# Optimization experiments

Hardware: AMD Instinct MI355X
Metric: run time of the kernel (lower is better)

The kernel has to match this reference:

```python
import jax, jax.numpy as jnp
import numpy as np

P = 8      # patch_size
DIM = 16   # per-head channel dim
HEADS = 4
LN_EPS = 1e-6


def _conv_patch(x, W, b):
    # stride=kernel=P patch conv; SAME degenerates to VALID when H%P==0
    y = jax.lax.conv_general_dilated(
        x, W, window_strides=(P, P), padding='VALID',
        dimension_numbers=('NHWC', 'HWIO', 'NHWC'))
    return y + b


def _proj_heads(x, W, b):
    # b h w (c p0 p1 head) -> b head (h p0) (w p1) c
    y = _conv_patch(x, W, b)
    B, hh, ww, _ = y.shape
    y = y.reshape(B, hh, ww, DIM, P, P, HEADS)
    y = y.transpose(0, 6, 1, 4, 2, 5, 3)            # b head hh p0 ww p1 c
    return y.reshape(B, HEADS, hh * P, ww * P, DIM)


def _to_patch(t):
    # n head (h p1) (w p2) c -> n head c h w p1 p2
    B, hd, H, W, c = t.shape
    t = t.reshape(B, hd, H // P, P, W // P, P, c)
    return t.transpose(0, 1, 6, 2, 4, 3, 5)


def _from_patch(t):
    # n head c h w p1 p2 -> n head (h p1) (w p2) c
    B, hd, c, hh, ww, _, _ = t.shape
    t = t.transpose(0, 1, 3, 5, 4, 6, 2)
    return t.reshape(B, hd, hh * P, ww * P, c)


def setup_inputs() -> dict:
    key = jax.random.key(0)
    ks = jax.random.split(key, 6)
    B, H, W, Cin = 4, 256, 256, 16
    feat = DIM * HEADS * P * P  # 4096
    s_qkv = 0.02
    inp = {
        'x': jax.random.normal(ks[0], (B, H, W, Cin), jnp.float32),
        'Wq': jax.random.normal(ks[1], (P, P, Cin, feat), jnp.float32) * s_qkv,
        'bq': jnp.zeros((feat,), jnp.float32),
        'Wk': jax.random.normal(ks[2], (P, P, Cin, feat), jnp.float32) * s_qkv,
        'bk': jnp.zeros((feat,), jnp.float32),
        'Wv': jax.random.normal(ks[3], (P, P, Cin, feat), jnp.float32) * s_qkv,
        'bv': jnp.zeros((feat,), jnp.float32),
        'ln_scale': jnp.ones((DIM,), jnp.float32),
        'ln_bias': jnp.zeros((DIM,), jnp.float32),
        'Wout': jax.random.normal(ks[4], (P, P, HEADS * DIM, DIM * P * P), jnp.float32) * 0.02,
        'bout': jnp.zeros((DIM * P * P,), jnp.float32),
    }
    return inp


def reference(x, Wq, bq, Wk, bk, Wv, bv, ln_scale, ln_bias, Wout, bout):
    q = _proj_heads(x, Wq, bq)  # [B, heads, H, W, dim]
    k = _proj_heads(x, Wk, bk)
    v = _proj_heads(x, Wv, bv)

    # frequency-domain 'attention': per-8x8-patch rfft2 multiply irfft2
    qf = jnp.fft.rfft2(_to_patch(q))
    kf = jnp.fft.rfft2(_to_patch(k))
    out = jnp.fft.irfft2(qf * kf, s=(P, P))
    out = _from_patch(out)                          # [B, heads, H, W, dim]

    # LayerNorm over channel dim (flax default eps=1e-6, scale+bias)
    mu = out.mean(-1, keepdims=True)
    var = ((out - mu) ** 2).mean(-1, keepdims=True)
    out = (out - mu) * jax.lax.rsqrt(var + LN_EPS) * ln_scale + ln_bias

    out = v * out
    # b head h w c -> b h w (head c)
    B, hd, H, W, c = out.shape
    out = out.transpose(0, 2, 3, 1, 4).reshape(B, H, W, hd * c)

    # output projection (no heads): conv then b h w (c p0 p1) -> b (h p0) (w p1) c
    y = _conv_patch(out, Wout, bout)
    Bo, hh, ww, _ = y.shape
    y = y.reshape(Bo, hh, ww, DIM, P, P).transpose(0, 1, 4, 2, 5, 3)
    return y.reshape(Bo, hh * P, ww * P, DIM)
```

## Files before the change

kernel.cpp:

```cpp
#include <hip/hip_runtime.h>
#include <hip/hip_bf16.h>
#include <cstdint>
#include <cstddef>

typedef float  f32x4  __attribute__((ext_vector_type(4)));
typedef __bf16 bf16x8 __attribute__((ext_vector_type(8)));
typedef __bf16 bf16x4 __attribute__((ext_vector_type(4)));


#define GLOAD_LDS16(gp, lp)                                                     \
    __builtin_amdgcn_global_load_lds(                                           \
        (const __attribute__((address_space(1))) void*)(gp),                    \
        (__attribute__((address_space(3))) void*)(lp), 16, 0, 0)

#define MFMA16(d, a, b) d = __builtin_amdgcn_mfma_f32_16x16x32_bf16(a, b, d, 0, 0, 0)

#define BAR() asm volatile("s_barrier" ::: "memory")

__global__ __launch_bounds__(256) void k_im2col(const float* __restrict__ x,
                                                __bf16* __restrict__ Xb)
{
    const int p = blockIdx.x;
    const int t = threadIdx.x;
    const int b = p >> 10, hh = (p >> 5) & 31, ww = p & 31;
    const int e = t * 4;
    const int c = e & 15, ij = e >> 4;
    const int i = ij >> 3, j = ij & 7;
    const size_t src = ((((size_t)(b * 256 + hh * 8 + i)) * 256) + (ww * 8 + j)) * 16 + c;
    f32x4 v = *(const f32x4*)(x + src);
    bf16x4 o;
    o[0] = (__bf16)v[0]; o[1] = (__bf16)v[1]; o[2] = (__bf16)v[2]; o[3] = (__bf16)v[3];
    *(bf16x4*)(Xb + (size_t)p * 1024 + e) = o;
}

__global__ __launch_bounds__(256) void k_wqkvT(const float* __restrict__ Wq,
                                               const float* __restrict__ Wk,
                                               const float* __restrict__ Wv,
                                               __bf16* __restrict__ WT)
{
    __shared__ float tile[64][261];
    int q = blockIdx.x;
    const int t = threadIdx.x;
    const int kb = q & 15;   q >>= 4;
    const int ch = q & 15;   q >>= 4;
    const int s  = q;
    const int k0 = kb * 64;
    const float* __restrict__ W = (s == 0) ? Wq : (s == 1) ? Wk : Wv;

#pragma unroll
    for (int rep = 0; rep < 16; rep++) {
        const int idx = rep * 256 + t;
        const int kl = idx >> 6, col4 = (idx & 63) * 4;
        const f32x4 v = *(const f32x4*)(W + (size_t)(k0 + kl) * 4096 + ch * 256 + col4);
        tile[kl][col4 + 0] = v[0];
        tile[kl][col4 + 1] = v[1];
        tile[kl][col4 + 2] = v[2];
        tile[kl][col4 + 3] = v[3];
    }
    __syncthreads();
    const size_t nbase = (size_t)s * 4096 + ch * 64;
#pragma unroll
    for (int rep = 0; rep < 64; rep++) {
        const int idx = rep * 256 + t;
        const int kl = idx & 63;
        const int rest = idx >> 6;
        const int p = rest & 63, h = rest >> 6;
        WT[(nbase + h * 1024 + p) * 1024 + k0 + kl] = (__bf16)tile[kl][p * 4 + h];
    }
}

__global__ __launch_bounds__(256) void k_biasperm(const float* __restrict__ bq,
                                                  const float* __restrict__ bk,
                                                  const float* __restrict__ bv,
                                                  float* __restrict__ bp)
{
    const int n = blockIdx.x * 256 + threadIdx.x;
    const int s = n >> 12;
    const int r = n & 4095;
    const int head = r >> 10, c = (r >> 6) & 15, pp = r & 63;
    const float* __restrict__ b = (s == 0) ? bq : (s == 1) ? bk : bv;
    bp[n] = b[c * 256 + pp * 4 + head];
}

__global__ __launch_bounds__(256) void k_woutT(const float* __restrict__ Wo,
                                               __bf16* __restrict__ WT)
{
    __shared__ float tile[64][129];
    const int q = blockIdx.x;
    const int t = threadIdx.x;
    const int n0 = (q & 15) * 64;
    const int k0 = (q >> 4) * 128;
    const int ch = n0 >> 6;
#pragma unroll
    for (int rep = 0; rep < 32; rep++) {
        const int idx = rep * 256 + t;
        const int kl = idx >> 6, nn = idx & 63;
        tile[nn][kl] = Wo[(size_t)(k0 + kl) * 1024 + n0 + nn];
    }
    __syncthreads();
#pragma unroll
    for (int rep = 0; rep < 32; rep++) {
        const int idx = rep * 256 + t;
        const int nn = idx >> 7, kl = idx & 127;
        const int no = ((nn >> 3) & 7) * 128 + (nn & 7) * 16 + ch;
        WT[(size_t)no * 4096 + k0 + kl] = (__bf16)tile[nn][kl];
    }
}

__device__ __forceinline__ void stage_half(const __bf16* __restrict__ mat,
                                           const int gRow0, const int K,
                                           const int k0, __bf16* lds, const int t)
{
    const int w6 = (t >> 6) << 6;
#pragma unroll
    for (int r = 0; r < 2; r++) {
        const int idx = r * 512 + t;
        const int row = idx >> 3;
        const int colb = ((t & 7) << 4) ^ ((row & 7) << 4);
        const char* gp = (const char*)(mat + (size_t)(gRow0 + row) * K + k0) + colb;
        GLOAD_LDS16(gp, (char*)lds + (size_t)(r * 512 + w6) * 16);
    }
}

__global__ __launch_bounds__(512, 1) void gemm256(const __bf16* __restrict__ A,
                                                  const __bf16* __restrict__ Bt,
                                                  __bf16* __restrict__ C,
                                                  const float* __restrict__ bias,
                                                  const int M, const int N,
                                                  const int K, const int nby)
{
    __shared__ __bf16 As[2][256 * 64];
    __shared__ __bf16 Bs[2][256 * 64];

    const int t = threadIdx.x;
    const int l = t & 63, w = t >> 6;
    const int wr = w >> 2, wc = w & 3;

    const int nwg = (int)gridDim.x, cpx = nwg >> 3;
    const int bid = (int)blockIdx.x;
    const int sbid = (bid & 7) * cpx + (bid >> 3);
    const int bm = sbid % nby, bn = sbid / nby;
    const int row0 = bm * 256, col0 = bn * 256;

    const int lrow = l & 15;
    const int lkb  = (l >> 4) << 4;
    const int lswz = (l & 7) << 4;
    const int ce0 = ((0  + lkb) ^ lswz) >> 1;
    const int ce1 = ((64 + lkb) ^ lswz) >> 1;

    const int arow = wr * 128 + lrow;
    const int brow = wc * 64 + lrow;

    const int NT = K >> 6;
    f32x4 acc[8][4] = {};
    bf16x8 a0[4][2], a1[4][2], b0[2][2], b1[2][2];

    stage_half(A,  row0,       K, 0,  As[0],        t);
    stage_half(A,  row0 + 128, K, 0,  As[0] + 8192, t);
    stage_half(A,  row0,       K, 64, As[1],        t);
    stage_half(A,  row0 + 128, K, 64, As[1] + 8192, t);
    stage_half(Bt, col0,       K, 0,  Bs[0],        t);
    stage_half(Bt, col0 + 128, K, 0,  Bs[0] + 8192, t);
    asm volatile("s_waitcnt vmcnt(0)" ::: "memory");
    BAR();
#pragma unroll
    for (int mi = 0; mi < 4; ++mi) {
        const int rr = (arow + mi * 16) * 64;
        a0[mi][0] = *(const bf16x8*)&As[0][rr + ce0];
        a0[mi][1] = *(const bf16x8*)&As[0][rr + ce1];
    }

    int cur = 0;
    for (int it = 0; it < NT; ++it) {
        const __bf16* AsC = As[cur];
        const __bf16* AsN = As[cur ^ 1];
        const __bf16* BsC = Bs[cur];
        __bf16* BsN = Bs[cur ^ 1];
        const bool stB = (it + 1 < NT);
        const bool stA = (it + 2 < NT);
        const bool pfA = (it + 1 < NT);
        const int kB = (it + 1) << 6;
        const int kA = (it + 2) << 6;

        BAR();
#pragma unroll
        for (int ni = 0; ni < 2; ++ni) {
            const int rr = (brow + ni * 16) * 64;
            b0[ni][0] = *(const bf16x8*)&BsC[rr + ce0];
            b0[ni][1] = *(const bf16x8*)&BsC[rr + ce1];
        }
#pragma unroll
        for (int ni = 0; ni < 2; ++ni) {
            const int rr = (brow + 32 + ni * 16) * 64;
            b1[ni][0] = *(const bf16x8*)&BsC[rr + ce0];
            b1[ni][1] = *(const bf16x8*)&BsC[rr + ce1];
        }
#pragma unroll
        for (int mi = 0; mi < 4; ++mi) {
            const int rr = (arow + 64 + mi * 16) * 64;
            a1[mi][0] = *(const bf16x8*)&AsC[rr + ce0];
            a1[mi][1] = *(const bf16x8*)&AsC[rr + ce1];
        }
        if (stB) stage_half(Bt, col0, K, kB, BsN, t);
        __builtin_amdgcn_s_setprio(1);
#pragma unroll
        for (int mi = 0; mi < 4; ++mi)
#pragma unroll
            for (int ni = 0; ni < 2; ++ni) {
                MFMA16(acc[mi][ni], a0[mi][0], b0[ni][0]);
                MFMA16(acc[mi][ni], a0[mi][1], b0[ni][1]);
            }
        __builtin_amdgcn_s_setprio(0);

        BAR();
        if (stB) stage_half(Bt, col0 + 128, K, kB, BsN + 8192, t);
        __builtin_amdgcn_s_setprio(1);
#pragma unroll
        for (int mi = 0; mi < 4; ++mi)
#pragma unroll
            for (int ni = 0; ni < 2; ++ni) {
                MFMA16(acc[mi][2 + ni], a0[mi][0], b1[ni][0]);
                MFMA16(acc[mi][2 + ni], a0[mi][1], b1[ni][1]);
            }
        __builtin_amdgcn_s_setprio(0);
        asm volatile("s_waitcnt vmcnt(4)" ::: "memory");

        BAR();
        if (pfA) {
#pragma unroll
            for (int mi = 0; mi < 4; ++mi) {
                const int rr = (arow + mi * 16) * 64;
                a0[mi][0] = *(const bf16x8*)&AsN[rr + ce0];
                a0[mi][1] = *(const bf16x8*)&AsN[rr + ce1];
            }
        }
        __builtin_amdgcn_s_setprio(1);
#pragma unroll
        for (int mi = 0; mi < 4; ++mi)
#pragma unroll
            for (int ni = 0; ni < 2; ++ni) {
                MFMA16(acc[4 + mi][ni], a1[mi][0], b0[ni][0]);
                MFMA16(acc[4 + mi][ni], a1[mi][1], b0[ni][1]);
            }
        __builtin_amdgcn_s_setprio(0);

        BAR();
        if (stA) {
            stage_half(A, row0,       K, kA, As[cur],        t);
            stage_half(A, row0 + 128, K, kA, As[cur] + 8192, t);
            asm volatile("s_waitcnt vmcnt(4)" ::: "memory");
        } else {
            asm volatile("s_waitcnt vmcnt(0)" ::: "memory");
        }
        __builtin_amdgcn_s_setprio(1);
#pragma unroll
        for (int mi = 0; mi < 4; ++mi)
#pragma unroll
            for (int ni = 0; ni < 2; ++ni) {
                MFMA16(acc[4 + mi][2 + ni], a1[mi][0], b1[ni][0]);
                MFMA16(acc[4 + mi][2 + ni], a1[mi][1], b1[ni][1]);
            }
        __builtin_amdgcn_s_setprio(0);

        cur ^= 1;
    }

    const int rbase = row0 + wr * 128;
    const int cbase = col0 + wc * 64;
    const int jr = (l >> 4) * 4;
#pragma unroll
    for (int m = 0; m < 8; ++m)
#pragma unroll
        for (int n = 0; n < 4; ++n) {
            const int cw = cbase + n * 16 + lrow;
            const float bsv = bias[cw];
#pragma unroll
            for (int j = 0; j < 4; ++j) {
                const int rw = rbase + m * 16 + jr + j;
                C[(size_t)rw * N + cw] = (__bf16)(acc[m][n][j] + bsv);
            }
        }
}

template <int BN>
__global__ __launch_bounds__(256, 3) void gemm_splitk(const __bf16* __restrict__ A,
                                                      const __bf16* __restrict__ Bt,
                                                      float* __restrict__ Pout,
                                                      const int K, const int kc)
{
    constexpr int BM  = 128, BK = 64;
    constexpr int NF  = BN / 32;
    constexpr int APW = (BM * BK / 512) / 4;
    constexpr int BPW = (BN * BK / 512) / 4;
    __shared__ __bf16 As[BM * BK];
    __shared__ __bf16 Bs[BN * BK];

    const int t = threadIdx.x;
    const int l = t & 63, w = t >> 6;

    const int nwg  = (int)gridDim.x;
    const int cpx  = nwg >> 3;
    const int bid  = (int)blockIdx.x;
    const int sbid = (bid & 7) * cpx + (bid >> 3);
    const int bm = sbid >> 4;
    const int ks = (sbid >> 3) & 1;
    const int bn = sbid & 7;
    const int row0 = bm * BM, col0 = bn * BN;
    const int kstart = ks * kc;

    const int wr = w >> 1, wc = w & 1;
    const int lr = l & 15;
    const int lk = (l >> 4) * 8;
    const int srow = l >> 3;
    const int scol = (l & 7) * 8;

    f32x4 acc[4][NF] = {};

    for (int k0 = kstart; k0 < kstart + kc; k0 += BK) {
        __syncthreads();
#pragma unroll
        for (int p = 0; p < APW; p++) {
            const int chunk = w * APW + p;
            const __bf16* gp = A + (size_t)(row0 + chunk * 8 + srow) * K + k0 + scol;
            GLOAD_LDS16(gp, &As[chunk * 512]);
        }
#pragma unroll
        for (int p = 0; p < BPW; p++) {
            const int chunk = w * BPW + p;
            const __bf16* gp = Bt + (size_t)(col0 + chunk * 8 + srow) * K + k0 + scol;
            GLOAD_LDS16(gp, &Bs[chunk * 512]);
        }
        __syncthreads();
#pragma unroll
        for (int kk = 0; kk < 2; kk++) {
            bf16x8 af[4], bfr[NF];
#pragma unroll
            for (int m = 0; m < 4; m++)
                af[m] = *(const bf16x8*)&As[(wr * 64 + m * 16 + lr) * BK + kk * 32 + lk];
#pragma unroll
            for (int n = 0; n < NF; n++)
                bfr[n] = *(const bf16x8*)&Bs[(wc * (BN / 2) + n * 16 + lr) * BK + kk * 32 + lk];
#pragma unroll
            for (int m = 0; m < 4; m++)
#pragma unroll
                for (int n = 0; n < NF; n++)
                    acc[m][n] = __builtin_amdgcn_mfma_f32_16x16x32_bf16(
                        af[m], bfr[n], acc[m][n], 0, 0, 0);
        }
    }

    float* __restrict__ P = Pout + (size_t)ks * 4194304;
    const int rbase = row0 + wr * 64;
    const int cbase = col0 + wc * (BN / 2);
#pragma unroll
    for (int m = 0; m < 4; m++)
#pragma unroll
        for (int n = 0; n < NF; n++) {
            const int cw = cbase + n * 16 + lr;
#pragma unroll
            for (int j = 0; j < 4; j++) {
                const int rw = rbase + m * 16 + (l >> 4) * 4 + j;
                P[(size_t)rw * 1024 + cw] = acc[m][n][j];
            }
        }
}

__global__ __launch_bounds__(256) void k_redscatter(const float* __restrict__ P,
                                                    const float* __restrict__ bo,
                                                    float* __restrict__ Y)
{
    const int i = (blockIdx.x * 256 + threadIdx.x) * 4;
    const int rw = i >> 10, cw = i & 1023;
    const f32x4 v0 = *(const f32x4*)(P + i);
    const f32x4 v1 = *(const f32x4*)(P + 4194304 + i);
    const int p0 = cw >> 7, low = cw & 127;
    const int b = rw >> 10, hh = (rw >> 5) & 31, wwp = rw & 31;
    float* dst = Y + (size_t)(b * 256 + hh * 8 + p0) * 4096 + wwp * 128 + low;
    f32x4 o;
#pragma unroll
    for (int j = 0; j < 4; j++) {
        const int c = cw + j;
        o[j] = v0[j] + v1[j] + bo[((c & 15) << 6) + ((c >> 7) << 3) + ((c >> 4) & 7)];
    }
    *(f32x4*)dst = o;
}

__global__ __launch_bounds__(128) void k_freqconv(const __bf16* __restrict__ C1,
                                                  const float* __restrict__ lns,
                                                  const float* __restrict__ lnb,
                                                  __bf16* __restrict__ Z)
{
    const int blk = blockIdx.x;
    const int p = blk >> 2, head = blk & 3;
    const int t = threadIdx.x;

    __shared__ float qs[16 * 68];
    __shared__ float ks[16 * 68];
    __shared__ float vs[16 * 68];
    __shared__ float os[16 * 68];

    const __bf16* __restrict__ base = C1 + (size_t)p * 12288 + head * 1024;
    {
        const int cl = t >> 3, off = (t & 7) * 8;
        const bf16x8 vq = *(const bf16x8*)(base + cl * 64 + off);
        const bf16x8 vk = *(const bf16x8*)(base + 4096 + cl * 64 + off);
        const bf16x8 vv = *(const bf16x8*)(base + 8192 + cl * 64 + off);
#pragma unroll
        for (int e = 0; e < 8; e++) {
            qs[cl * 68 + off + e] = (float)vq[e];
            ks[cl * 68 + off + e] = (float)vk[e];
            vs[cl * 68 + off + e] = (float)vv[e];
        }
    }
    __syncthreads();

    const int cc = t >> 3, p0 = t & 7;
    float outr[8] = {0.f, 0.f, 0.f, 0.f, 0.f, 0.f, 0.f, 0.f};
#pragma unroll
    for (int i0 = 0; i0 < 8; i0++) {
        const int kr = (p0 - i0) & 7;
        const f32x4 qa = *(const f32x4*)&qs[cc * 68 + i0 * 8];
        const f32x4 qb = *(const f32x4*)&qs[cc * 68 + i0 * 8 + 4];
        const f32x4 ka = *(const f32x4*)&ks[cc * 68 + kr * 8];
        const f32x4 kb = *(const f32x4*)&ks[cc * 68 + kr * 8 + 4];
        const float qrow[8] = {qa[0], qa[1], qa[2], qa[3], qb[0], qb[1], qb[2], qb[3]};
        const float krow[8] = {ka[0], ka[1], ka[2], ka[3], kb[0], kb[1], kb[2], kb[3]};
#pragma unroll
        for (int j = 0; j < 8; j++) {
            const float qv = qrow[j];
#pragma unroll
            for (int p1 = 0; p1 < 8; p1++)
                outr[p1] = fmaf(qv, krow[(p1 - j) & 7], outr[p1]);
        }
    }
#pragma unroll
    for (int e = 0; e < 8; e++)
        os[cc * 68 + p0 * 8 + e] = outr[e];
    __syncthreads();

    if (t < 64) {
        const int pp = t;
        float o[16];
        float mu = 0.f;
#pragma unroll
        for (int c2 = 0; c2 < 16; c2++) { o[c2] = os[c2 * 68 + pp]; mu += o[c2]; }
        mu *= 0.0625f;
        float var = 0.f;
#pragma unroll
        for (int c2 = 0; c2 < 16; c2++) { const float d = o[c2] - mu; var = fmaf(d, d, var); }
        var *= 0.0625f;
        const float rs = rsqrtf(var + 1e-6f);
        bf16x8 z0, z1;
#pragma unroll
        for (int c2 = 0; c2 < 16; c2++) {
            float zv = (o[c2] - mu) * rs * lns[c2] + lnb[c2];
            zv *= vs[c2 * 68 + pp];
            if (c2 < 8) z0[c2] = (__bf16)zv; else z1[c2 - 8] = (__bf16)zv;
        }
        bf16x8* zp = (bf16x8*)(Z + (size_t)p * 4096 + pp * 64 + head * 16);
        zp[0] = z0;
        zp[1] = z1;
    }
}

extern "C" void kernel_launch(void* const* d_in, const int* in_sizes, int n_in,
                              void* d_out, int out_size, void* d_ws, size_t ws_size,
                              hipStream_t stream)
{
    const float* x   = (const float*)d_in[0];
    const float* Wq  = (const float*)d_in[1];
    const float* bq  = (const float*)d_in[2];
    const float* Wk  = (const float*)d_in[3];
    const float* bk  = (const float*)d_in[4];
    const float* Wv  = (const float*)d_in[5];
    const float* bv  = (const float*)d_in[6];
    const float* lns = (const float*)d_in[7];
    const float* lnb = (const float*)d_in[8];
    const float* Wo  = (const float*)d_in[9];
    const float* bo  = (const float*)d_in[10];
    float* out = (float*)d_out;

    char* ws = (char*)d_ws;
    __bf16* Xb    = (__bf16*)(ws);
    __bf16* WqkvT = (__bf16*)(ws + 8388608);
    float*  bperm = (float*) (ws + 33554432);
    __bf16* WoutT = (__bf16*)(ws + 33603584);
    __bf16* C1    = (__bf16*)(ws + 41992192);
    __bf16* Z     = (__bf16*)(ws + 142655488);
    float*  Ppart = (float*) (ws + 41992192);

    k_im2col  <<<dim3(4096), dim3(256), 0, stream>>>(x, Xb);
    k_wqkvT   <<<dim3(768),  dim3(256), 0, stream>>>(Wq, Wk, Wv, WqkvT);
    k_biasperm<<<dim3(48),   dim3(256), 0, stream>>>(bq, bk, bv, bperm);
    k_woutT   <<<dim3(512),  dim3(256), 0, stream>>>(Wo, WoutT);

    gemm256<<<dim3(768), dim3(512), 0, stream>>>(Xb, WqkvT, C1, bperm,
                                                 4096, 12288, 1024, 16);

    k_freqconv<<<dim3(16384), dim3(128), 0, stream>>>(C1, lns, lnb, Z);

    gemm_splitk<128><<<dim3(512), dim3(256), 0, stream>>>(Z, WoutT, Ppart,
                                                          4096, 2048);

    k_redscatter<<<dim3(4096), dim3(256), 0, stream>>>(Ppart, bo, out);
}
```

Baseline: 232.4 us.

## Restructure GEMM main loop from four to two phases per K-tile

Merges the four quarter-tile MFMA phases of the bf16 GEMM main loop into two half-tile phases. All B fragments are loaded once, and both B half-stages are issued together. This removes two barriers per iteration and moves the vmcnt waits. The cost is more live B registers and coarser interleaving of global-to-LDS loads with MFMA work, which could raise register pressure or expose load latency.

```diff
diff --git a/kernel.cpp b/kernel.cpp
--- a/kernel.cpp
+++ b/kernel.cpp
@@ -153,7 +153,7 @@
 
     const int NT = K >> 6;
     f32x4 acc[8][4] = {};
-    bf16x8 a0[4][2], a1[4][2], b0[2][2], b1[2][2];
+    bf16x8 a0[4][2], a1[4][2], b[4][2];
 
     stage_half(A,  row0,       K, 0,  As[0],        t);
     stage_half(A,  row0 + 128, K, 0,  As[0] + 8192, t);
@@ -184,16 +184,10 @@
 
         BAR();
 #pragma unroll
-        for (int ni = 0; ni < 2; ++ni) {
+        for (int ni = 0; ni < 4; ++ni) {
             const int rr = (brow + ni * 16) * 64;
-            b0[ni][0] = *(const bf16x8*)&BsC[rr + ce0];
-            b0[ni][1] = *(const bf16x8*)&BsC[rr + ce1];
-        }
-#pragma unroll
-        for (int ni = 0; ni < 2; ++ni) {
-            const int rr = (brow + 32 + ni * 16) * 64;
-            b1[ni][0] = *(const bf16x8*)&BsC[rr + ce0];
-            b1[ni][1] = *(const bf16x8*)&BsC[rr + ce1];
+            b[ni][0] = *(const bf16x8*)&BsC[rr + ce0];
+            b[ni][1] = *(const bf16x8*)&BsC[rr + ce1];
         }
 #pragma unroll
         for (int mi = 0; mi < 4; ++mi) {
@@ -201,29 +195,21 @@
             a1[mi][0] = *(const bf16x8*)&AsC[rr + ce0];
             a1[mi][1] = *(const bf16x8*)&AsC[rr + ce1];
         }
-        if (stB) stage_half(Bt, col0, K, kB, BsN, t);
+        if (stB) {
+            stage_half(Bt, col0,       K, kB, BsN,        t);
+            stage_half(Bt, col0 + 128, K, kB, BsN + 8192, t);
+        }
         __builtin_amdgcn_s_setprio(1);
 #pragma unroll
         for (int mi = 0; mi < 4; ++mi)
 #pragma unroll
-            for (int ni = 0; ni < 2; ++ni) {
-                MFMA16(acc[mi][ni], a0[mi][0], b0[ni][0]);
-                MFMA16(acc[mi][ni], a0[mi][1], b0[ni][1]);
+            for (int ni = 0; ni < 4; ++ni) {
+                MFMA16(acc[mi][ni], a0[mi][0], b[ni][0]);
+                MFMA16(acc[mi][ni], a0[mi][1], b[ni][1]);
             }
         __builtin_amdgcn_s_setprio(0);
-
-        BAR();
-        if (stB) stage_half(Bt, col0 + 128, K, kB, BsN + 8192, t);
-        __builtin_amdgcn_s_setprio(1);
-#pragma unroll
-        for (int mi = 0; mi < 4; ++mi)
-#pragma unroll
-            for (int ni = 0; ni < 2; ++ni) {
-                MFMA16(acc[mi][2 + ni], a0[mi][0], b1[ni][0]);
-                MFMA16(acc[mi][2 + ni], a0[mi][1], b1[ni][1]);
-            }
-        __builtin_amdgcn_s_setprio(0);
-        asm volatile("s_waitcnt vmcnt(4)" ::: "memory");
+        if (pfA)
+            asm volatile("s_waitcnt vmcnt(4)" ::: "memory");
 
         BAR();
         if (pfA) {
@@ -234,33 +220,23 @@
                 a0[mi][1] = *(const bf16x8*)&AsN[rr + ce1];
             }
         }
-        __builtin_amdgcn_s_setprio(1);
-#pragma unroll
-        for (int mi = 0; mi < 4; ++mi)
-#pragma unroll
-            for (int ni = 0; ni < 2; ++ni) {
-                MFMA16(acc[4 + mi][ni], a1[mi][0], b0[ni][0]);
-                MFMA16(acc[4 + mi][ni], a1[mi][1], b0[ni][1]);
-            }
-        __builtin_amdgcn_s_setprio(0);
-
-        BAR();
         if (stA) {
             stage_half(A, row0,       K, kA, As[cur],        t);
             stage_half(A, row0 + 128, K, kA, As[cur] + 8192, t);
-            asm volatile("s_waitcnt vmcnt(4)" ::: "memory");
-        } else {
-            asm volatile("s_waitcnt vmcnt(0)" ::: "memory");
         }
         __builtin_amdgcn_s_setprio(1);
 #pragma unroll
         for (int mi = 0; mi < 4; ++mi)
 #pragma unroll
-            for (int ni = 0; ni < 2; ++ni) {
-                MFMA16(acc[4 + mi][2 + ni], a1[mi][0], b1[ni][0]);
-                MFMA16(acc[4 + mi][2 + ni], a1[mi][1], b1[ni][1]);
+            for (int ni = 0; ni < 4; ++ni) {
+                MFMA16(acc[4 + mi][ni], a1[mi][0], b[ni][0]);
+                MFMA16(acc[4 + mi][ni], a1[mi][1], b[ni][1]);
             }
         __builtin_amdgcn_s_setprio(0);
+        if (stB) {
+            if (stA) asm volatile("s_waitcnt vmcnt(4)" ::: "memory");
+            else     asm volatile("s_waitcnt vmcnt(0)" ::: "memory");
+        }
 
         cur ^= 1;
     }
```

Result: no change. 231.7 us (-0.3%).
